# Kernel optimization log

Hardware: AMD Instinct MI355X
Metric: run time of the kernel (lower is better)

The kernel has to match this reference:

```python
import jax, jax.numpy as jnp
import numpy as np

# Coefficient form of the 16 differentiable binary logic ops:
# op(a,b) = c0 + c1*a + c2*b + c3*a*b  (algebraically identical to bin_op_s's stacked einsum)
_COEF_NP = np.array([
    [0, 0, 0, 0],    # 0: zeros
    [0, 0, 0, 1],    # 1: a*b
    [0, 1, 0, -1],   # 2: a*(1-b)
    [0, 1, 0, 0],    # 3: a
    [0, 0, 1, -1],   # 4: (1-a)*b
    [0, 0, 1, 0],    # 5: b
    [0, 1, 1, -2],   # 6: xor
    [0, 1, 1, -1],   # 7: or
    [1, -1, -1, 1],  # 8: nor
    [1, -1, -1, 2],  # 9: xnor
    [1, 0, -1, 0],   # 10: 1-b
    [1, 0, -1, 1],   # 11: b=>a
    [1, -1, 0, 0],   # 12: 1-a
    [1, -1, 0, 1],   # 13: a=>b
    [1, 0, 0, -1],   # 14: nand
    [1, 0, 0, 0],    # 15: ones
], dtype=np.float32)
COEF = jnp.asarray(_COEF_NP)

TREE_DEPTH = 3
NUM_CLASSES = 10
TAU = 10.0
K = 32
BATCH = 128


def _conv_tree(x, leaf_idx, w):
    # x: [B,C,H,W]; leaf_idx: [O,8] int32 into C*9 unfolded patch dim; w: [O,7,16]
    B, C, H, W = x.shape
    xp = jnp.pad(x, ((0, 0), (0, 0), (1, 1), (1, 1)))
    # unfold (kernel=3, stride=1, pad=1): torch ordering is c*9 + spatial
    pats = jnp.stack([xp[:, :, di:di + H, dj:dj + W]
                      for di in range(3) for dj in range(3)], axis=2)  # [B,C,9,H,W]
    pats = pats.reshape(B, C * 9, H * W).transpose(0, 2, 1)            # [B,L,C*9]
    cur = pats[:, :, leaf_idx]                                         # [B,L,O,8]
    sw = jax.nn.softmax(w, axis=-1)                                    # training-mode soft gates
    coef = jnp.einsum('ogk,kc->ogc', sw, COEF)                         # [O,7,4]
    for level in range(TREE_DEPTH):
        a = cur[..., 0::2]
        b = cur[..., 1::2]                                             # [B,L,O,n]
        n = a.shape[-1]
        off = 2 ** level - 1                                           # faithful to original gate indexing
        c = coef[:, off:off + n]                                       # [O,n,4]
        cur = c[..., 0] + c[..., 1] * a + c[..., 2] * b + c[..., 3] * (a * b)
    out = cur[..., 0]                                                  # [B,L,O]
    return out.transpose(0, 2, 1).reshape(B, -1, H, W)


def _orpool(x):
    B, C, H, W = x.shape
    return x.reshape(B, C, H // 2, 2, W // 2, 2).max(axis=(3, 5))


def _difflogic(x, ca, cb, w):
    # x: [B,D]; ca/cb: [O]; w: [O,16]
    a = x[:, ca]
    b = x[:, cb]
    c = jax.nn.softmax(w, axis=-1) @ COEF                              # [O,4]
    return c[:, 0] + c[:, 1] * a + c[:, 2] * b + c[:, 3] * (a * b)


def _forward(x, w1, w2, w3, w4, fw1, fw2, fw3,
             l1, l2, l3, l4, ca1, cb1, ca2, cb2, ca3, cb3):
    # threshold-encode to 9 binary channels (bilinear resize to 32x32 is identity here)
    xb = jnp.concatenate([(x > (i + 1) / 4).astype(jnp.float32) for i in range(3)], axis=1)
    h = xb
    for li, w in ((l1, w1), (l2, w2), (l3, w3), (l4, w4)):
        h = _orpool(_conv_tree(h, li, w))
    h = h.reshape(h.shape[0], -1)                                      # [B, 4096]
    h = _difflogic(h, ca1, cb1, fw1)
    h = _difflogic(h, ca2, cb2, fw2)
    h = _difflogic(h, ca3, cb3, fw3)
    return h.reshape(h.shape[0], NUM_CLASSES, -1).sum(-1) / TAU


def _make_leaf_idx(in_ch, out_ch, rng):
    idx = np.zeros((out_ch, 8), np.int32)
    for c in range(out_ch):
        chans = rng.permutation(in_ch)[:2]
        parts = [ch * 9 + rng.permutation(9)[:4] for ch in chans]
        idx[c] = np.concatenate(parts)
    return jnp.asarray(idx)


def _unique_connections(in_dim, out_dim, rng):
    x = np.arange(in_dim, dtype=np.int64)
    a, b = x[::2], x[1::2]
    m = min(len(a), len(b)); a, b = a[:m], b[:m]
    if len(a) < out_dim:
        a = np.concatenate([a, x[1::2]]); b = np.concatenate([b, x[2::2]])
        m = min(len(a), len(b)); a, b = a[:m], b[:m]
    offset = 2
    while out_dim > len(a) > offset:
        a = np.concatenate([a, x[:-offset]]); b = np.concatenate([b, x[offset:]])
        offset += 1
    a, b = a[:out_dim], b[:out_dim]
    perm = rng.permutation(out_dim)
    return jnp.asarray(a[perm]), jnp.asarray(b[perm])


def setup_inputs() -> dict:
    key = jax.random.key(0)
    rng = np.random.default_rng(0)
    ks = jax.random.split(key, 8)
    x = jax.random.uniform(ks[0], (BATCH, 3, 32, 32), dtype=jnp.float32)
    chans = [(9, K), (K, 4 * K), (4 * K, 16 * K), (16 * K, 32 * K)]
    w1, w2, w3, w4 = [jax.random.normal(ks[1 + i], (oc, 7, 16), dtype=jnp.float32)
                      for i, (_, oc) in enumerate(chans)]
    l1, l2, l3, l4 = [_make_leaf_idx(ic, oc, rng) for ic, oc in chans]
    fc_in = 32 * K * 4
    fdims = [(fc_in, 1280 * K), (1280 * K, 640 * K), (640 * K, 320 * K)]
    fw1, fw2, fw3 = [jax.random.normal(ks[5 + i], (od, 16), dtype=jnp.float32)
                     for i, (_, od) in enumerate(fdims)]
    (ca1, cb1), (ca2, cb2), (ca3, cb3) = [_unique_connections(i, o, rng) for i, o in fdims]
    return dict(x=x, w1=w1, w2=w2, w3=w3, w4=w4, fw1=fw1, fw2=fw2, fw3=fw3,
                l1=l1, l2=l2, l3=l3, l4=l4,
                ca1=ca1, cb1=cb1, ca2=ca2, cb2=cb2, ca3=ca3, cb3=cb3)


def reference(x, w1, w2, w3, w4, fw1, fw2, fw3,
              l1, l2, l3, l4, ca1, cb1, ca2, cb2, ca3, cb3):
    return _forward(x, w1, w2, w3, w4, fw1, fw2, fw3,
                    l1, l2, l3, l4, ca1, cb1, ca2, cb2, ca3, cb3)
```

## Files before the change

### kernel.cpp

```cpp
#include <hip/hip_runtime.h>
#include <math.h>


typedef _Float16 h16;
typedef _Float16 h2 __attribute__((ext_vector_type(2)));

__constant__ float c_coef_tbl[16][4] = {
    {0, 0, 0, 0}, {0, 0, 0, 1}, {0, 1, 0, -1}, {0, 1, 0, 0},
    {0, 0, 1, -1}, {0, 0, 1, 0}, {0, 1, 1, -2}, {0, 1, 1, -1},
    {1, -1, -1, 1}, {1, -1, -1, 2}, {1, 0, -1, 0}, {1, 0, -1, 1},
    {1, -1, 0, 0}, {1, -1, 0, 1}, {1, 0, 0, -1}, {1, 0, 0, 0}};

__device__ __forceinline__ float4 softmax_coef(const float* __restrict__ wr) {
  float m = -1e30f;
#pragma unroll
  for (int k = 0; k < 16; ++k) m = fmaxf(m, wr[k]);
  float e[16], s = 0.f;
#pragma unroll
  for (int k = 0; k < 16; ++k) { e[k] = __expf(wr[k] - m); s += e[k]; }
  float inv = 1.f / s;
  float c0 = 0.f, c1 = 0.f, c2 = 0.f, c3 = 0.f;
#pragma unroll
  for (int k = 0; k < 16; ++k) {
    c0 += e[k] * c_coef_tbl[k][0];
    c1 += e[k] * c_coef_tbl[k][1];
    c2 += e[k] * c_coef_tbl[k][2];
    c3 += e[k] * c_coef_tbl[k][3];
  }
  return make_float4(c0 * inv, c1 * inv, c2 * inv, c3 * inv);
}

__device__ __forceinline__ float gate_eval(float4 c, float a, float b) {
  return c.x + c.y * a + c.z * b + c.w * (a * b);
}
__device__ __forceinline__ float4 dec_cf(uint2 u) {
  h2 p0, p1;
  *(unsigned*)&p0 = u.x;
  *(unsigned*)&p1 = u.y;
  return make_float4((float)p0[0], (float)p0[1], (float)p1[0], (float)p1[1]);
}
__device__ __forceinline__ h2 gateh(const h2* c, h2 a, h2 b) {
  return c[0] + c[1] * a + c[2] * b + c[3] * (a * b);
}

__global__ void prep_all(const float* __restrict__ w1, const float* __restrict__ w2,
                         const float* __restrict__ w3, const float* __restrict__ w4,
                         const float* __restrict__ fw1, const float* __restrict__ fw2,
                         const float* __restrict__ fw3,
                         const int* __restrict__ ca1, const int* __restrict__ cb1,
                         const int* __restrict__ ca2, const int* __restrict__ cb2,
                         const int* __restrict__ ca3, const int* __restrict__ cb3,
                         float4* __restrict__ coefC,
                         unsigned short* __restrict__ midx16,
                         _Float16* __restrict__ mcoefh) {
  int g = blockIdx.x * blockDim.x + threadIdx.x;
  if (g < 71680) {
    int o = g / 7;
    int s = g - o * 7;
    float4 c;
    if (s < 4) {
      int k = (s < 2) ? ca3[o] : cb3[o];
      int j = (s & 1) ? cb2[k] : ca2[k];
      midx16[o * 8 + s * 2]     = (unsigned short)ca1[j];
      midx16[o * 8 + s * 2 + 1] = (unsigned short)cb1[j];
      c = softmax_coef(fw1 + j * 16);
    } else if (s < 6) {
      int k = (s == 4) ? ca3[o] : cb3[o];
      c = softmax_coef(fw2 + k * 16);
    } else {
      c = softmax_coef(fw3 + o * 16);
    }
    _Float16* mc = mcoefh + o * 28 + s * 4;
    mc[0] = (_Float16)c.x; mc[1] = (_Float16)c.y;
    mc[2] = (_Float16)c.z; mc[3] = (_Float16)c.w;
  } else if (g < 78464) {
    int gg = g - 71680;
    int base = gg;
    const float* w;
    if (gg < 128)       {             w = w1; }
    else if (gg < 640)  { gg -= 128;  w = w2; }
    else if (gg < 2688) { gg -= 640;  w = w3; }
    else                { gg -= 2688; w = w4; }
    coefC[base] = softmax_coef(w + ((gg >> 2) * 7 + (gg & 3)) * 16);
  }
}

template <int C, int H, int W, int OC, int IPS, int OPS, bool OUTDUP>
__device__ void stage(const h2* __restrict__ in, h2* __restrict__ outD,
                      h16* __restrict__ outP,
                      const int* __restrict__ leaf,
                      const float4* __restrict__ coef, int tid) {
  constexpr int Wp = W + 2;
  constexpr int PH = H / 2, PW = W / 2;
  constexpr int NPOS = PH * PW;
  constexpr int TPO = 1024 / OC;
  constexpr int ITER = NPOS / TPO;
  constexpr int OWp = PW + 2;

  int oc = tid / TPO;
  int lane = tid % TPO;

  int toff[8];
#pragma unroll
  for (int l = 0; l < 8; ++l) {
    int k = leaf[oc * 8 + l];
    int cc = k / 9;
    int p = k - 9 * cc;
    int di = p / 3;
    int dj = p - 3 * di;
    toff[l] = cc * IPS + di * Wp + dj;
  }
  h2 ch[4][4];
#pragma unroll
  for (int r = 0; r < 4; ++r) {
    float4 c = coef[oc * 4 + r];
    _Float16 x0 = (_Float16)c.x, x1 = (_Float16)c.y,
             x2 = (_Float16)c.z, x3 = (_Float16)c.w;
    ch[r][0][0] = x0; ch[r][0][1] = x0;
    ch[r][1][0] = x1; ch[r][1][1] = x1;
    ch[r][2][0] = x2; ch[r][2][1] = x2;
    ch[r][3][0] = x3; ch[r][3][1] = x3;
  }

#pragma unroll
  for (int it = 0; it < ITER; ++it) {
    int pos = lane + it * TPO;
    int pw = pos % PW, ph = pos / PW;
    h2 o01[2];
#pragma unroll
    for (int py = 0; py < 2; ++py) {
      int pbase = (2 * ph + py) * Wp + 2 * pw;
      h2 lv[8];
#pragma unroll
      for (int l = 0; l < 8; ++l) lv[l] = in[toff[l] + pbase];
      h2 t0 = gateh(ch[0], lv[0], lv[1]);
      h2 t1 = gateh(ch[1], lv[2], lv[3]);
      h2 t2 = gateh(ch[2], lv[4], lv[5]);
      h2 t3 = gateh(ch[3], lv[6], lv[7]);
      h2 u0 = gateh(ch[1], t0, t1);
      h2 u1 = gateh(ch[2], t2, t3);
      o01[py] = gateh(ch[3], u0, u1);
    }
    _Float16 m0 = o01[0][0] > o01[1][0] ? o01[0][0] : o01[1][0];
    _Float16 m1 = o01[0][1] > o01[1][1] ? o01[0][1] : o01[1][1];
    _Float16 v = m0 > m1 ? m0 : m1;
    if (OUTDUP) {
      h16* oh = (h16*)outD;
      int cell = oc * OPS + (ph + 1) * OWp + (pw + 1);
      oh[2 * cell] = v;
      oh[2 * cell - 1] = v;
    } else {
      outP[oc * NPOS + ph * PW + pw] = v;
    }
  }
}

__global__ __launch_bounds__(1024) void mega(
    const float* __restrict__ x, const float4* __restrict__ coefC,
    const int* __restrict__ l1, const int* __restrict__ l2,
    const int* __restrict__ l3, const int* __restrict__ l4,
    const unsigned short* __restrict__ midx16,
    const _Float16* __restrict__ mcoefh, float* __restrict__ out) {
  __shared__ __align__(16) h2 XB[9 * 1157];
  __shared__ __align__(16) h2 S1[32 * 325];
  __shared__ __align__(16) h2 S2[128 * 101];
  __shared__ __align__(16) h16 S3[512 * 16];
  __shared__ __align__(16) h16 S4[1024 * 4];
  __shared__ float red[16][10];
  int tid = threadIdx.x;
  int b = blockIdx.x;

  {
    float4* z1 = (float4*)S1;
    float4* z2 = (float4*)S2;
    float4 zz = make_float4(0.f, 0.f, 0.f, 0.f);
    for (int i = tid; i < 2600; i += 1024) z1[i] = zz;
    for (int i = tid; i < 3232; i += 1024) z2[i] = zz;
  }
  const float* xg = x + b * 3072;
  for (int cell = tid; cell < 9 * 1157; cell += 1024) {
    int c9 = cell / 1157;
    int rem = cell - c9 * 1157;
    if (rem >= 1156) continue;
    int i = rem / 34, j = rem - 34 * (rem / 34);
    int th = c9 / 3, c = c9 - 3 * th;
    float thr = (float)(th + 1) * 0.25f;
    _Float16 lo = (_Float16)0, hi = (_Float16)0;
    if (i >= 1 && i <= 32) {
      const float* row = xg + c * 1024 + (i - 1) * 32;
      if (j >= 1 && j <= 32) lo = (_Float16)((row[j - 1] > thr) ? 1.f : 0.f);
      if (j <= 31)           hi = (_Float16)((row[j] > thr) ? 1.f : 0.f);
    }
    XB[cell] = h2{lo, hi};
  }
  __syncthreads();

  stage<9, 32, 32, 32, 1157, 325, true>(XB, S1, nullptr, l1, coefC, tid);
  __syncthreads();
  stage<32, 16, 16, 128, 325, 101, true>(S1, S2, nullptr, l2, coefC + 128, tid);
  __syncthreads();
  stage<128, 8, 8, 512, 101, 0, false>(S2, nullptr, S3, l3, coefC + 640, tid);
  __syncthreads();

  {
    int oc = tid;
    int cc[8], di[8], dj[8];
#pragma unroll
    for (int l = 0; l < 8; ++l) {
      int k = l4[oc * 8 + l];
      cc[l] = k / 9;
      int p = k - 9 * cc[l];
      di[l] = p / 3;
      dj[l] = p - 3 * di[l];
    }
    float4 c0 = coefC[2688 + oc * 4 + 0];
    float4 c1 = coefC[2688 + oc * 4 + 1];
    float4 c2 = coefC[2688 + oc * 4 + 2];
    float4 c3 = coefC[2688 + oc * 4 + 3];
#pragma unroll
    for (int pos = 0; pos < 4; ++pos) {
      int pw = pos & 1, ph = pos >> 1;
      float best = -1e30f;
#pragma unroll
      for (int py = 0; py < 2; ++py) {
#pragma unroll
        for (int px = 0; px < 2; ++px) {
          int i = 2 * ph + py, j = 2 * pw + px;
          float lv[8];
#pragma unroll
          for (int l = 0; l < 8; ++l) {
            int ii = i + di[l] - 1, jj = j + dj[l] - 1;
            float v = 0.f;
            if ((unsigned)ii < 4u && (unsigned)jj < 4u)
              v = (float)S3[cc[l] * 16 + ii * 4 + jj];
            lv[l] = v;
          }
          float t0 = gate_eval(c0, lv[0], lv[1]);
          float t1 = gate_eval(c1, lv[2], lv[3]);
          float t2 = gate_eval(c2, lv[4], lv[5]);
          float t3 = gate_eval(c3, lv[6], lv[7]);
          float u0 = gate_eval(c1, t0, t1);
          float u1 = gate_eval(c2, t2, t3);
          best = fmaxf(best, gate_eval(c3, u0, u1));
        }
      }
      S4[oc * 4 + pos] = (h16)best;
    }
  }
  __syncthreads();

  const uint4* mi = (const uint4*)midx16;
  const uint2* mc = (const uint2*)mcoefh;
  int wid = tid >> 6;
#pragma unroll
  for (int k = 0; k < 10; ++k) {
    int o = k * 1024 + tid;
    uint4 I = mi[o];
    const uint2* cfp = mc + o * 7;
    float L0 = gate_eval(dec_cf(cfp[0]), (float)S4[I.x & 0xffff], (float)S4[I.x >> 16]);
    float L1 = gate_eval(dec_cf(cfp[1]), (float)S4[I.y & 0xffff], (float)S4[I.y >> 16]);
    float L2 = gate_eval(dec_cf(cfp[2]), (float)S4[I.z & 0xffff], (float)S4[I.z >> 16]);
    float L3 = gate_eval(dec_cf(cfp[3]), (float)S4[I.w & 0xffff], (float)S4[I.w >> 16]);
    float M0 = gate_eval(dec_cf(cfp[4]), L0, L1);
    float M1 = gate_eval(dec_cf(cfp[5]), L2, L3);
    float y = gate_eval(dec_cf(cfp[6]), M0, M1);
#pragma unroll
    for (int m = 32; m > 0; m >>= 1) y += __shfl_xor(y, m, 64);
    if ((tid & 63) == 0) red[wid][k] = y;
  }
  __syncthreads();
  if (tid < 10) {
    float s = 0.f;
#pragma unroll
    for (int w = 0; w < 16; ++w) s += red[w][tid];
    out[b * 10 + tid] = s * 0.1f;
  }
}

extern "C" void kernel_launch(void* const* d_in, const int* in_sizes, int n_in,
                              void* d_out, int out_size, void* d_ws, size_t ws_size,
                              hipStream_t stream) {
  const float* x   = (const float*)d_in[0];
  const float* w1  = (const float*)d_in[1];
  const float* w2  = (const float*)d_in[2];
  const float* w3  = (const float*)d_in[3];
  const float* w4  = (const float*)d_in[4];
  const float* fw1 = (const float*)d_in[5];
  const float* fw2 = (const float*)d_in[6];
  const float* fw3 = (const float*)d_in[7];
  const int* l1  = (const int*)d_in[8];
  const int* l2  = (const int*)d_in[9];
  const int* l3  = (const int*)d_in[10];
  const int* l4  = (const int*)d_in[11];
  const int* ca1 = (const int*)d_in[12];
  const int* cb1 = (const int*)d_in[13];
  const int* ca2 = (const int*)d_in[14];
  const int* cb2 = (const int*)d_in[15];
  const int* ca3 = (const int*)d_in[16];
  const int* cb3 = (const int*)d_in[17];

  char* ws = (char*)d_ws;
  float4*         coefC  = (float4*)ws;
  unsigned short* midx16 = (unsigned short*)(ws + 108544);
  _Float16*       mcoefh = (_Float16*)(ws + 108544 + 163840);

  prep_all<<<307, 256, 0, stream>>>(w1, w2, w3, w4, fw1, fw2, fw3,
                                    ca1, cb1, ca2, cb2, ca3, cb3,
                                    coefC, midx16, mcoefh);
  mega<<<128, 1024, 0, stream>>>(x, coefC, l1, l2, l3, l4, midx16, mcoefh,
                                 (float*)d_out);
}
```

Measured before the change: 63.14 us.

## Remap conv stages to wave-per-channel with shuffle-based vertical pooling

Replaces the templated conv stage with per-stage code where each wave owns one output channel and lane pairs handle the two rows of a pool window. Vertical max-pooling is done with a lane shuffle instead of both rows being computed by one thread. Each thread now evaluates two horizontally adjacent packed pairs per load. Padded row strides change (35/19/11) to reduce LDS bank conflicts, and S4 is aliased onto the XB buffer to cut shared-memory footprint, which may raise occupancy. This adds shuffle overhead and more complex indexing.

```diff
diff --git a/kernel.cpp b/kernel.cpp
--- a/kernel.cpp
+++ b/kernel.cpp
@@ -41,6 +41,26 @@
 }
 __device__ __forceinline__ h2 gateh(const h2* c, h2 a, h2 b) {
   return c[0] + c[1] * a + c[2] * b + c[3] * (a * b);
+}
+__device__ __forceinline__ h2 tree8(const h2 (&ch)[4][4], const h2* lv) {
+  h2 t0 = gateh(ch[0], lv[0], lv[1]);
+  h2 t1 = gateh(ch[1], lv[2], lv[3]);
+  h2 t2 = gateh(ch[2], lv[4], lv[5]);
+  h2 t3 = gateh(ch[3], lv[6], lv[7]);
+  h2 u0 = gateh(ch[1], t0, t1);
+  h2 u1 = gateh(ch[2], t2, t3);
+  return gateh(ch[3], u0, u1);
+}
+__device__ __forceinline__ h2 shfl1_h2(h2 v) {
+  int a = __builtin_bit_cast(int, v);
+  int b = __shfl_xor(a, 1, 64);
+  return __builtin_bit_cast(h2, b);
+}
+__device__ __forceinline__ h2 pkmax(h2 a, h2 b) {
+  h2 r;
+  r[0] = a[0] > b[0] ? a[0] : b[0];
+  r[1] = a[1] > b[1] ? a[1] : b[1];
+  return r;
 }
 
 __global__ void prep_all(const float* __restrict__ w1, const float* __restrict__ w2,
@@ -85,22 +105,10 @@
   }
 }
 
-template <int C, int H, int W, int OC, int IPS, int OPS, bool OUTDUP>
-__device__ void stage(const h2* __restrict__ in, h2* __restrict__ outD,
-                      h16* __restrict__ outP,
-                      const int* __restrict__ leaf,
-                      const float4* __restrict__ coef, int tid) {
-  constexpr int Wp = W + 2;
-  constexpr int PH = H / 2, PW = W / 2;
-  constexpr int NPOS = PH * PW;
-  constexpr int TPO = 1024 / OC;
-  constexpr int ITER = NPOS / TPO;
-  constexpr int OWp = PW + 2;
-
-  int oc = tid / TPO;
-  int lane = tid % TPO;
-
-  int toff[8];
+__device__ __forceinline__ void load_oc(const int* __restrict__ leaf,
+                                        const float4* __restrict__ coef, int oc,
+                                        int IPS, int IRS, int (&toff)[8],
+                                        h2 (&ch)[4][4]) {
 #pragma unroll
   for (int l = 0; l < 8; ++l) {
     int k = leaf[oc * 8 + l];
@@ -108,9 +116,8 @@
     int p = k - 9 * cc;
     int di = p / 3;
     int dj = p - 3 * di;
-    toff[l] = cc * IPS + di * Wp + dj;
-  }
-  h2 ch[4][4];
+    toff[l] = cc * IPS + di * IRS + dj;
+  }
 #pragma unroll
   for (int r = 0; r < 4; ++r) {
     float4 c = coef[oc * 4 + r];
@@ -121,38 +128,6 @@
     ch[r][2][0] = x2; ch[r][2][1] = x2;
     ch[r][3][0] = x3; ch[r][3][1] = x3;
   }
-
-#pragma unroll
-  for (int it = 0; it < ITER; ++it) {
-    int pos = lane + it * TPO;
-    int pw = pos % PW, ph = pos / PW;
-    h2 o01[2];
-#pragma unroll
-    for (int py = 0; py < 2; ++py) {
-      int pbase = (2 * ph + py) * Wp + 2 * pw;
-      h2 lv[8];
-#pragma unroll
-      for (int l = 0; l < 8; ++l) lv[l] = in[toff[l] + pbase];
-      h2 t0 = gateh(ch[0], lv[0], lv[1]);
-      h2 t1 = gateh(ch[1], lv[2], lv[3]);
-      h2 t2 = gateh(ch[2], lv[4], lv[5]);
-      h2 t3 = gateh(ch[3], lv[6], lv[7]);
-      h2 u0 = gateh(ch[1], t0, t1);
-      h2 u1 = gateh(ch[2], t2, t3);
-      o01[py] = gateh(ch[3], u0, u1);
-    }
-    _Float16 m0 = o01[0][0] > o01[1][0] ? o01[0][0] : o01[1][0];
-    _Float16 m1 = o01[0][1] > o01[1][1] ? o01[0][1] : o01[1][1];
-    _Float16 v = m0 > m1 ? m0 : m1;
-    if (OUTDUP) {
-      h16* oh = (h16*)outD;
-      int cell = oc * OPS + (ph + 1) * OWp + (pw + 1);
-      oh[2 * cell] = v;
-      oh[2 * cell - 1] = v;
-    } else {
-      outP[oc * NPOS + ph * PW + pw] = v;
-    }
-  }
 }
 
 __global__ __launch_bounds__(1024) void mega(
@@ -161,45 +136,122 @@
     const int* __restrict__ l3, const int* __restrict__ l4,
     const unsigned short* __restrict__ midx16,
     const _Float16* __restrict__ mcoefh, float* __restrict__ out) {
-  __shared__ __align__(16) h2 XB[9 * 1157];
-  __shared__ __align__(16) h2 S1[32 * 325];
-  __shared__ __align__(16) h2 S2[128 * 101];
+  __shared__ __align__(16) h2 XB[9 * 1190];
+  __shared__ __align__(16) h2 S1[32 * 342];
+  __shared__ __align__(16) h2 S2[128 * 111];
   __shared__ __align__(16) h16 S3[512 * 16];
-  __shared__ __align__(16) h16 S4[1024 * 4];
   __shared__ float red[16][10];
+  h16* S4h = (h16*)XB;
+
   int tid = threadIdx.x;
   int b = blockIdx.x;
+  int wave = tid >> 6, lane = tid & 63;
+  int py = lane & 1, halfl = lane >> 1;
 
   {
     float4* z1 = (float4*)S1;
     float4* z2 = (float4*)S2;
     float4 zz = make_float4(0.f, 0.f, 0.f, 0.f);
-    for (int i = tid; i < 2600; i += 1024) z1[i] = zz;
-    for (int i = tid; i < 3232; i += 1024) z2[i] = zz;
+    for (int i = tid; i < 2736; i += 1024) z1[i] = zz;
+    for (int i = tid; i < 3552; i += 1024) z2[i] = zz;
   }
   const float* xg = x + b * 3072;
-  for (int cell = tid; cell < 9 * 1157; cell += 1024) {
-    int c9 = cell / 1157;
-    int rem = cell - c9 * 1157;
-    if (rem >= 1156) continue;
-    int i = rem / 34, j = rem - 34 * (rem / 34);
+  for (int cell = tid; cell < 10710; cell += 1024) {
+    int c9 = cell / 1190;
+    int rem = cell - c9 * 1190;
+    int r = rem / 35, cj = rem - 35 * r;
     int th = c9 / 3, c = c9 - 3 * th;
     float thr = (float)(th + 1) * 0.25f;
     _Float16 lo = (_Float16)0, hi = (_Float16)0;
-    if (i >= 1 && i <= 32) {
-      const float* row = xg + c * 1024 + (i - 1) * 32;
-      if (j >= 1 && j <= 32) lo = (_Float16)((row[j - 1] > thr) ? 1.f : 0.f);
-      if (j <= 31)           hi = (_Float16)((row[j] > thr) ? 1.f : 0.f);
+    if (r >= 1 && r <= 32 && cj <= 34) {
+      const float* row = xg + c * 1024 + (r - 1) * 32;
+      if (cj >= 1 && cj <= 32) lo = (_Float16)((row[cj - 1] > thr) ? 1.f : 0.f);
+      if (cj <= 31)            hi = (_Float16)((row[cj] > thr) ? 1.f : 0.f);
     }
     XB[cell] = h2{lo, hi};
   }
   __syncthreads();
 
-  stage<9, 32, 32, 32, 1157, 325, true>(XB, S1, nullptr, l1, coefC, tid);
-  __syncthreads();
-  stage<32, 16, 16, 128, 325, 101, true>(S1, S2, nullptr, l2, coefC + 128, tid);
-  __syncthreads();
-  stage<128, 8, 8, 512, 101, 0, false>(S2, nullptr, S3, l3, coefC + 640, tid);
+#pragma unroll
+  for (int k = 0; k < 2; ++k) {
+    int oc = wave + 16 * k;
+    int toff[8]; h2 ch[4][4];
+    load_oc(l1, coefC, oc, 1190, 35, toff, ch);
+#pragma unroll
+    for (int it = 0; it < 4; ++it) {
+      int pairIdx = it * 32 + halfl;
+      int pwp = pairIdx & 7, ph = pairIdx >> 3;
+      int base = (2 * ph + py) * 35 + 4 * pwp;
+      h2 A[8], B[8];
+#pragma unroll
+      for (int l = 0; l < 8; ++l) { int a0 = toff[l] + base; A[l] = XB[a0]; B[l] = XB[a0 + 2]; }
+      h2 oA = tree8(ch, A), oB = tree8(ch, B);
+      h2 pA = pkmax(oA, shfl1_h2(oA));
+      h2 pB = pkmax(oB, shfl1_h2(oB));
+      _Float16 vA = pA[0] > pA[1] ? pA[0] : pA[1];
+      _Float16 vB = pB[0] > pB[1] ? pB[0] : pB[1];
+      if (py == 0) {
+        int rowc = oc * 342 + (ph + 1) * 19 + 2 * pwp;
+        S1[rowc + 1] = h2{vA, vB};
+        h16* s1h = (h16*)S1;
+        s1h[2 * rowc + 1] = vA;
+        s1h[2 * (rowc + 2)] = vB;
+      }
+    }
+  }
+  __syncthreads();
+
+  {
+    int pwp = halfl & 3, ph = halfl >> 2;
+    int base = (2 * ph + py) * 19 + 4 * pwp;
+#pragma unroll
+    for (int k = 0; k < 8; ++k) {
+      int oc = wave + 16 * k;
+      int toff[8]; h2 ch[4][4];
+      load_oc(l2, coefC + 128, oc, 342, 19, toff, ch);
+      h2 A[8], B[8];
+#pragma unroll
+      for (int l = 0; l < 8; ++l) { int a0 = toff[l] + base; A[l] = S1[a0]; B[l] = S1[a0 + 2]; }
+      h2 oA = tree8(ch, A), oB = tree8(ch, B);
+      h2 pA = pkmax(oA, shfl1_h2(oA));
+      h2 pB = pkmax(oB, shfl1_h2(oB));
+      _Float16 vA = pA[0] > pA[1] ? pA[0] : pA[1];
+      _Float16 vB = pB[0] > pB[1] ? pB[0] : pB[1];
+      if (py == 0) {
+        int rowc = oc * 111 + (ph + 1) * 11 + 2 * pwp;
+        S2[rowc + 1] = h2{vA, vB};
+        h16* s2h = (h16*)S2;
+        s2h[2 * rowc + 1] = vA;
+        s2h[2 * (rowc + 2)] = vB;
+      }
+    }
+  }
+  __syncthreads();
+
+  {
+    int q = lane >> 4, ll = lane & 15;
+    int py3 = ll & 1;
+    int pairIdx = ll >> 1;
+    int pwp = pairIdx & 1, ph = pairIdx >> 1;
+    int base = (2 * ph + py3) * 11 + 4 * pwp;
+#pragma unroll
+    for (int it = 0; it < 8; ++it) {
+      int oc = it * 64 + wave * 4 + q;
+      int toff[8]; h2 ch[4][4];
+      load_oc(l3, coefC + 640, oc, 111, 11, toff, ch);
+      h2 A[8], B[8];
+#pragma unroll
+      for (int l = 0; l < 8; ++l) { int a0 = toff[l] + base; A[l] = S2[a0]; B[l] = S2[a0 + 2]; }
+      h2 oA = tree8(ch, A), oB = tree8(ch, B);
+      h2 pA = pkmax(oA, shfl1_h2(oA));
+      h2 pB = pkmax(oB, shfl1_h2(oB));
+      _Float16 vA = pA[0] > pA[1] ? pA[0] : pA[1];
+      _Float16 vB = pB[0] > pB[1] ? pB[0] : pB[1];
+      if (py3 == 0) {
+        ((h2*)S3)[(oc * 16 + ph * 4 + 2 * pwp) >> 1] = h2{vA, vB};
+      }
+    }
+  }
   __syncthreads();
 
   {
@@ -222,10 +274,10 @@
       int pw = pos & 1, ph = pos >> 1;
       float best = -1e30f;
 #pragma unroll
-      for (int py = 0; py < 2; ++py) {
+      for (int pyy = 0; pyy < 2; ++pyy) {
 #pragma unroll
         for (int px = 0; px < 2; ++px) {
-          int i = 2 * ph + py, j = 2 * pw + px;
+          int i = 2 * ph + pyy, j = 2 * pw + px;
           float lv[8];
 #pragma unroll
           for (int l = 0; l < 8; ++l) {
@@ -244,7 +296,7 @@
           best = fmaxf(best, gate_eval(c3, u0, u1));
         }
       }
-      S4[oc * 4 + pos] = (h16)best;
+      S4h[oc * 4 + pos] = (h16)best;
     }
   }
   __syncthreads();
@@ -257,10 +309,10 @@
     int o = k * 1024 + tid;
     uint4 I = mi[o];
     const uint2* cfp = mc + o * 7;
-    float L0 = gate_eval(dec_cf(cfp[0]), (float)S4[I.x & 0xffff], (float)S4[I.x >> 16]);
-    float L1 = gate_eval(dec_cf(cfp[1]), (float)S4[I.y & 0xffff], (float)S4[I.y >> 16]);
-    float L2 = gate_eval(dec_cf(cfp[2]), (float)S4[I.z & 0xffff], (float)S4[I.z >> 16]);
-    float L3 = gate_eval(dec_cf(cfp[3]), (float)S4[I.w & 0xffff], (float)S4[I.w >> 16]);
+    float L0 = gate_eval(dec_cf(cfp[0]), (float)S4h[I.x & 0xffff], (float)S4h[I.x >> 16]);
+    float L1 = gate_eval(dec_cf(cfp[1]), (float)S4h[I.y & 0xffff], (float)S4h[I.y >> 16]);
+    float L2 = gate_eval(dec_cf(cfp[2]), (float)S4h[I.z & 0xffff], (float)S4h[I.z >> 16]);
+    float L3 = gate_eval(dec_cf(cfp[3]), (float)S4h[I.w & 0xffff], (float)S4h[I.w >> 16]);
     float M0 = gate_eval(dec_cf(cfp[4]), L0, L1);
     float M1 = gate_eval(dec_cf(cfp[5]), L2, L3);
     float y = gate_eval(dec_cf(cfp[6]), M0, M1);
```

After: 65.15 us. +3.2%, slower.

## Split FC stage out of conv megakernel into wide per-class kernel

Applied to the files above, without the earlier changes.

The fully connected difflogic tail moves out of the 128-block conv megakernel into a separate kernel with 1280 blocks, one per batch element and class. The conv kernel now writes its layer-4 activations to a global workspace. The goal is to spread the FC work's gather-heavy loads of indices and coefficients across many more CUs than the 128 blocks allowed. The cost is one extra launch and a round-trip of activations through global memory.

```diff
diff --git a/kernel.cpp b/kernel.cpp
--- a/kernel.cpp
+++ b/kernel.cpp
@@ -159,14 +159,11 @@
     const float* __restrict__ x, const float4* __restrict__ coefC,
     const int* __restrict__ l1, const int* __restrict__ l2,
     const int* __restrict__ l3, const int* __restrict__ l4,
-    const unsigned short* __restrict__ midx16,
-    const _Float16* __restrict__ mcoefh, float* __restrict__ out) {
+    h16* __restrict__ s4g) {
   __shared__ __align__(16) h2 XB[9 * 1157];
   __shared__ __align__(16) h2 S1[32 * 325];
   __shared__ __align__(16) h2 S2[128 * 101];
   __shared__ __align__(16) h16 S3[512 * 16];
-  __shared__ __align__(16) h16 S4[1024 * 4];
-  __shared__ float red[16][10];
   int tid = threadIdx.x;
   int b = blockIdx.x;
 
@@ -217,6 +214,7 @@
     float4 c1 = coefC[2688 + oc * 4 + 1];
     float4 c2 = coefC[2688 + oc * 4 + 2];
     float4 c3 = coefC[2688 + oc * 4 + 3];
+    h16 vout[4];
 #pragma unroll
     for (int pos = 0; pos < 4; ++pos) {
       int pw = pos & 1, ph = pos >> 1;
@@ -244,17 +242,40 @@
           best = fmaxf(best, gate_eval(c3, u0, u1));
         }
       }
-      S4[oc * 4 + pos] = (h16)best;
-    }
+      vout[pos] = (h16)best;
+    }
+    uint2 pack;
+    h2 plo{vout[0], vout[1]}, phi{vout[2], vout[3]};
+    pack.x = __builtin_bit_cast(unsigned, plo);
+    pack.y = __builtin_bit_cast(unsigned, phi);
+    *(uint2*)(s4g + b * 4096 + oc * 4) = pack;
+  }
+}
+
+__global__ __launch_bounds__(256) void fc_kernel(
+    const h16* __restrict__ s4g,
+    const unsigned short* __restrict__ midx16,
+    const _Float16* __restrict__ mcoefh, float* __restrict__ out) {
+  __shared__ __align__(16) h16 S4[4096];
+  __shared__ float red[4];
+  int tid = threadIdx.x;
+  int b = blockIdx.x / 10;
+  int cls = blockIdx.x - b * 10;
+
+  {
+    const uint4* src = (const uint4*)(s4g + b * 4096);
+    uint4* dst = (uint4*)S4;
+    dst[tid] = src[tid];
+    dst[tid + 256] = src[tid + 256];
   }
   __syncthreads();
 
   const uint4* mi = (const uint4*)midx16;
   const uint2* mc = (const uint2*)mcoefh;
-  int wid = tid >> 6;
-#pragma unroll
-  for (int k = 0; k < 10; ++k) {
-    int o = k * 1024 + tid;
+  float ysum = 0.f;
+#pragma unroll
+  for (int t = 0; t < 4; ++t) {
+    int o = cls * 1024 + t * 256 + tid;
     uint4 I = mi[o];
     const uint2* cfp = mc + o * 7;
     float L0 = gate_eval(dec_cf(cfp[0]), (float)S4[I.x & 0xffff], (float)S4[I.x >> 16]);
@@ -263,18 +284,14 @@
     float L3 = gate_eval(dec_cf(cfp[3]), (float)S4[I.w & 0xffff], (float)S4[I.w >> 16]);
     float M0 = gate_eval(dec_cf(cfp[4]), L0, L1);
     float M1 = gate_eval(dec_cf(cfp[5]), L2, L3);
-    float y = gate_eval(dec_cf(cfp[6]), M0, M1);
-#pragma unroll
-    for (int m = 32; m > 0; m >>= 1) y += __shfl_xor(y, m, 64);
-    if ((tid & 63) == 0) red[wid][k] = y;
-  }
-  __syncthreads();
-  if (tid < 10) {
-    float s = 0.f;
-#pragma unroll
-    for (int w = 0; w < 16; ++w) s += red[w][tid];
-    out[b * 10 + tid] = s * 0.1f;
-  }
+    ysum += gate_eval(dec_cf(cfp[6]), M0, M1);
+  }
+#pragma unroll
+  for (int m = 32; m > 0; m >>= 1) ysum += __shfl_xor(ysum, m, 64);
+  if ((tid & 63) == 0) red[tid >> 6] = ysum;
+  __syncthreads();
+  if (tid == 0)
+    out[b * 10 + cls] = (red[0] + red[1] + red[2] + red[3]) * 0.1f;
 }
 
 extern "C" void kernel_launch(void* const* d_in, const int* in_sizes, int n_in,
@@ -302,11 +319,12 @@
   char* ws = (char*)d_ws;
   float4*         coefC  = (float4*)ws;
   unsigned short* midx16 = (unsigned short*)(ws + 108544);
-  _Float16*       mcoefh = (_Float16*)(ws + 108544 + 163840);
+  _Float16*       mcoefh = (_Float16*)(ws + 272384);
+  h16*            s4g    = (h16*)(ws + 845824);
 
   prep_all<<<307, 256, 0, stream>>>(w1, w2, w3, w4, fw1, fw2, fw3,
                                     ca1, cb1, ca2, cb2, ca3, cb3,
                                     coefC, midx16, mcoefh);
-  mega<<<128, 1024, 0, stream>>>(x, coefC, l1, l2, l3, l4, midx16, mcoefh,
-                                 (float*)d_out);
-}
+  mega<<<128, 1024, 0, stream>>>(x, coefC, l1, l2, l3, l4, s4g);
+  fc_kernel<<<1280, 256, 0, stream>>>(s4g, midx16, mcoefh, (float*)d_out);
+}
```

Measured after the change: 85.42 us. +35.3%, slower.
